# Performance work log

Measured on AMD Instinct MI355X. Metric: run time of the kernel, lower is better.

The kernel has to match this reference:

```python
import jax, jax.numpy as jnp
import numpy as np

N = 256          # Preisach mesh resolution
M = 4096         # number of applied-field time steps
H_MIN = -1.0
H_MAX = 1.0
B_SAT = 1.0


def setup_inputs() -> dict:
    key = jax.random.key(0)
    k1, k2 = jax.random.split(key)
    # applied magnetic field trace H_1..H_t in [0, 1)
    h = jax.random.uniform(k1, (M,), dtype=jnp.float32)
    # raw (pre-softplus) hysteresis density vector, length n(n+1)/2
    raw_density = jax.random.normal(k2, (N * (N + 1) // 2,), dtype=jnp.float32)
    # generate_asym_mesh equivalent: beta (xx) varies along columns,
    # alpha (yy) along rows; tril keeps the alpha >= beta Preisach triangle.
    lin = jnp.linspace(H_MIN, H_MAX, N, dtype=jnp.float32)
    xx, yy = jnp.meshgrid(lin, lin)
    return {"h": h, "raw_density": raw_density, "xx": xx, "yy": yy}


def _update_states(h, xx, yy):
    # hs = [-h_min, H_1, ..., H_t]
    hs = jnp.concatenate([jnp.full((1,), -H_MIN, dtype=h.dtype), h])
    # faithful to torch: at i=0, hs[i-1] wraps to the LAST element hs[-1]
    prev = jnp.concatenate([hs[-1:], hs[:-1]])
    init = -jnp.ones_like(xx)  # all hysterons start 'off'

    def step(state, hp_h):
        hp, hc = hp_h
        swept_up = jnp.where(yy >= hc, state, 1.0)    # sweep up: flip on below alpha=h
        swept_dn = jnp.where(xx <= hc, state, -1.0)   # sweep left: flip off above beta=h
        new = jnp.where(hc > hp, swept_up,
                        jnp.where(hc < hp, swept_dn, state))
        new = jnp.tril(new)
        return new, new

    _, states = jax.lax.scan(step, init, (prev, hs))
    return states  # (M+1, N, N)


def reference(h, raw_density, xx, yy):
    n = xx.shape[0]
    states = _update_states(h, xx, yy)
    # softplus density, scattered into lower-triangular matrix (vector_to_tril)
    dens_vec = jax.nn.softplus(raw_density)
    dens = jnp.zeros((n, n), dtype=dens_vec.dtype).at[jnp.tril_indices(n)].set(dens_vec)
    a = B_SAT / jnp.sum(dens)
    # b[i] = sum(dens * states[i+1])  -> single contraction over mesh dims
    b = jnp.einsum('tij,ij->t', states[1:], dens)
    return b * a
```

## Files before the change

kernel.cpp:

```cpp
#include <hip/hip_runtime.h>
#include <hip/hip_bf16.h>


#define NN 256
#define MM 4096
#define LSTEPS 16
#define NCHUNK (MM / LSTEPS)


__device__ __forceinline__ int rowOff(int i) { return i * (i + 3) / 2; }

__global__ __launch_bounds__(NN) void k_prep(const float* __restrict__ raw,
                                             const float* __restrict__ h,
                                             const float* __restrict__ lin,
                                             float* __restrict__ pref,
                                             int* __restrict__ codes,
                                             int* __restrict__ agg) {
    int tid = threadIdx.x;
    if (blockIdx.x < NN) {
        int i = blockIdx.x;
        float sp = 0.f;
        if (tid <= i) {
            float x = raw[i * (i + 1) / 2 + tid];
            sp = (x > 20.f) ? x : log1pf(expf(x));
        }
        float v = sp;
        int lane = tid & 63, wid = tid >> 6;
        #pragma unroll
        for (int o = 1; o < 64; o <<= 1) {
            float n = __shfl_up(v, o);
            if (lane >= o) v += n;
        }
        __shared__ float wsum[4];
        if (lane == 63) wsum[wid] = v;
        __syncthreads();
        float off = 0.f;
        for (int w = 0; w < wid; ++w) off += wsum[w];
        v += off;
        int base = rowOff(i);
        if (tid == 0) pref[base] = 0.f;
        if (tid <= i) pref[base + tid + 1] = v;
    } else {
        __shared__ float slin[NN];
        slin[tid] = lin[tid];
        __syncthreads();
        int k = (blockIdx.x - NN) * NN + tid;
        float hc = h[k];
        float hp = (k == 0) ? 1.0f : h[k - 1];
        double td = ((double)hc + 1.0) * 127.5;
        int code;
        if (hc > hp) {
            int g = (int)ceil(td);
            while (g < NN && slin[g] < hc) ++g;
            while (g > 0 && slin[g - 1] >= hc) --g;
            code = (g << 16) | 0xFFFF;
        } else if (hc < hp) {
            int g = (int)floor(td) + 1;
            while (g < NN && slin[g] <= hc) ++g;
            while (g > 0 && slin[g - 1] > hc) --g;
            code = g;
        } else {
            code = 0xFFFF;
        }
        codes[k] = code;
        int iup = code >> 16, jdn = code & 0xFFFF;
        #pragma unroll
        for (int m = 1; m < 16; m <<= 1) {
            iup = max(iup, __shfl_xor(iup, m));
            jdn = min(jdn, __shfl_xor(jdn, m));
        }
        if ((tid & 15) == 0) agg[k >> 4] = (iup << 16) | jdn;
    }
}

__global__ __launch_bounds__(NN) void k_main(const int* __restrict__ codes,
                                             const int* __restrict__ aggG,
                                             const float* __restrict__ pref,
                                             float* __restrict__ out) {
    __shared__ __align__(16) int sc[MM];
    __shared__ __align__(16) int sagg[NCHUNK];
    __shared__ float sPart[LSTEPS + 1][4];
    int tid = threadIdx.x;
    const int i = tid;
    const int T = blockIdx.x * LSTEPS;

    int base = rowOff(i);
    float rowtot = pref[base + i + 1];

    {
        const int4* g4 = (const int4*)codes;
        int4* d4 = (int4*)sc;
        #pragma unroll
        for (int u = 0; u < MM / 4 / NN; ++u) d4[tid + u * NN] = g4[tid + u * NN];
        sagg[tid] = aggG[tid];
    }
    __syncthreads();

    int runmin = i + 1;
    int c = (i == NN - 1) ? 0 : i + 1;
    bool done = (i == NN - 1);
    const int4* s4 = (const int4*)sc;
    const int4* a4 = (const int4*)sagg;
    const int jlim = blockIdx.x - 1;
    for (int jb = (jlim >> 4) << 4; jb >= 0; jb -= 16) {
        if (__all(done)) break;
        int4 A0 = a4[jb / 4 + 0];
        int4 A1 = a4[jb / 4 + 1];
        int4 A2 = a4[jb / 4 + 2];
        int4 A3 = a4[jb / 4 + 3];
        int ag[16] = { A0.x, A0.y, A0.z, A0.w, A1.x, A1.y, A1.z, A1.w,
                       A2.x, A2.y, A2.z, A2.w, A3.x, A3.y, A3.z, A3.w };
        #pragma unroll
        for (int u = 0; u < 16; ++u) if (jb + u > jlim) ag[u] = 0xFFFF;
        bool anyw = false; int bmin = 0xFFFF;
        #pragma unroll
        for (int u = 0; u < 16; ++u) {
            anyw = anyw || (!done && (i < (ag[u] >> 16)));
            bmin = min(bmin, ag[u] & 0xFFFF);
        }
        if (__any(anyw)) {
            #pragma unroll
            for (int u = 15; u >= 0; --u) {
                int a = ag[u];
                bool want = !done && (i < (a >> 16));
                if (__any(want)) {
                    int q = jb + u;
                    int4 w0 = s4[q * 4 + 0];
                    int4 w1 = s4[q * 4 + 1];
                    int4 w2 = s4[q * 4 + 2];
                    int4 w3 = s4[q * 4 + 3];
                    int cb[16] = { w0.x, w0.y, w0.z, w0.w, w1.x, w1.y, w1.z, w1.w,
                                   w2.x, w2.y, w2.z, w2.w, w3.x, w3.y, w3.z, w3.w };
                    #pragma unroll
                    for (int s = 15; s >= 0; --s) {
                        int code = cb[s];
                        bool cover = i < (code >> 16);
                        runmin = min(runmin, code & 0xFFFF);
                        c = (cover && !done) ? runmin : c;
                        done = done || cover;
                    }
                } else {
                    runmin = min(runmin, a & 0xFFFF);
                }
            }
        } else {
            runmin = min(runmin, bmin);
        }
    }
    if (!done) c = runmin;

    int4 f0 = s4[blockIdx.x * 4 + 0];
    int4 f1 = s4[blockIdx.x * 4 + 1];
    int4 f2 = s4[blockIdx.x * 4 + 2];
    int4 f3 = s4[blockIdx.x * 4 + 3];
    int fc[16] = { f0.x, f0.y, f0.z, f0.w, f1.x, f1.y, f1.z, f1.w,
                   f2.x, f2.y, f2.z, f2.w, f3.x, f3.y, f3.z, f3.w };
    float vals[LSTEPS];
    #pragma unroll
    for (int kk = 0; kk < LSTEPS; ++kk) {
        int code = fc[kk];
        c = (i < (code >> 16)) ? (i + 1) : min(c, code & 0xFFFF);
        vals[kk] = pref[base + c];
    }
    #pragma unroll
    for (int kk = 0; kk <= LSTEPS; ++kk) {
        float v = (kk < LSTEPS) ? vals[kk] : rowtot;
        v += __shfl_xor(v, 1);  v += __shfl_xor(v, 2);  v += __shfl_xor(v, 4);
        v += __shfl_xor(v, 8);  v += __shfl_xor(v, 16); v += __shfl_xor(v, 32);
        if ((tid & 63) == 0) sPart[kk][tid >> 6] = v;
    }
    __syncthreads();
    if (tid < LSTEPS) {
        float s  = sPart[tid][0] + sPart[tid][1] + sPart[tid][2] + sPart[tid][3];
        float st = sPart[LSTEPS][0] + sPart[LSTEPS][1] + sPart[LSTEPS][2] + sPart[LSTEPS][3];
        out[T + tid] = (2.f * s - st) / st;
    }
}

extern "C" void kernel_launch(void* const* d_in, const int* in_sizes, int n_in,
                              void* d_out, int out_size, void* d_ws, size_t ws_size,
                              hipStream_t stream) {
    const float* h   = (const float*)d_in[0];
    const float* raw = (const float*)d_in[1];
    const float* xx  = (const float*)d_in[2];

    int*   codes = (int*)d_ws;
    int*   agg   = (int*)((char*)d_ws + 16384);
    float* pref  = (float*)((char*)d_ws + 17408);

    k_prep<<<NN + MM / NN, NN, 0, stream>>>(raw, h, xx, pref, codes, agg);
    k_main<<<MM / LSTEPS, NN, 0, stream>>>(codes, agg, pref, (float*)d_out);
}
```

Baseline: 69.86 us.

## Replace backward scan with precomputed per-row composable chunk operators

Each row's state transition over a chunk of 16 steps is encoded as a composable operator (a reset flag plus a running min). The prep kernel precomputes these operators per chunk and per superchunk. The main kernel then composes at most about 31 operators to get the initial state. This replaces the data-dependent backward search with early exits, removes staging all 4096 codes into shared memory, and shrinks shared-memory use. The cost is extra global reads of the operator tables and more work in the prep kernel.

```diff
diff --git a/kernel.cpp b/kernel.cpp
--- a/kernel.cpp
+++ b/kernel.cpp
@@ -1,21 +1,29 @@
 #include <hip/hip_runtime.h>
-#include <hip/hip_bf16.h>
 
 
 #define NN 256
 #define MM 4096
 #define LSTEPS 16
 #define NCHUNK (MM / LSTEPS)
+#define NSUP   (NCHUNK / 16)
+#define IDENT  0xFFFF
 
 
 __device__ __forceinline__ int rowOff(int i) { return i * (i + 3) / 2; }
+
+__device__ __forceinline__ int opcompose(int a, int b) {
+    int m = min(a & 0xFFFF, b & 0xFFFF);
+    int r = (a & 0x10000) | m;
+    return (b & 0x10000) ? b : r;
+}
 
 __global__ __launch_bounds__(NN) void k_prep(const float* __restrict__ raw,
                                              const float* __restrict__ h,
                                              const float* __restrict__ lin,
                                              float* __restrict__ pref,
                                              int* __restrict__ codes,
-                                             int* __restrict__ agg) {
+                                             int* __restrict__ sup,
+                                             int4* __restrict__ cho) {
     int tid = threadIdx.x;
     if (blockIdx.x < NN) {
         int i = blockIdx.x;
@@ -42,9 +50,11 @@
         if (tid <= i) pref[base + tid + 1] = v;
     } else {
         __shared__ float slin[NN];
+        __shared__ __align__(16) int scodes[NN];
         slin[tid] = lin[tid];
         __syncthreads();
-        int k = (blockIdx.x - NN) * NN + tid;
+        int e = blockIdx.x - NN;
+        int k = e * NN + tid;
         float hc = h[k];
         float hp = (k == 0) ? 1.0f : h[k - 1];
         double td = ((double)hc + 1.0) * 127.5;
@@ -63,102 +73,84 @@
             code = 0xFFFF;
         }
         codes[k] = code;
-        int iup = code >> 16, jdn = code & 0xFFFF;
+        scodes[tid] = code;
+        __syncthreads();
+
+        const int i = tid;
+        const int4* s4 = (const int4*)scodes;
+        int cop[16];
         #pragma unroll
-        for (int m = 1; m < 16; m <<= 1) {
-            iup = max(iup, __shfl_xor(iup, m));
-            jdn = min(jdn, __shfl_xor(jdn, m));
+        for (int u = 0; u < 16; ++u) {
+            int4 q0 = s4[u * 4 + 0];
+            int4 q1 = s4[u * 4 + 1];
+            int4 q2 = s4[u * 4 + 2];
+            int4 q3 = s4[u * 4 + 3];
+            int cb[16] = { q0.x, q0.y, q0.z, q0.w, q1.x, q1.y, q1.z, q1.w,
+                           q2.x, q2.y, q2.z, q2.w, q3.x, q3.y, q3.z, q3.w };
+            int run = IDENT;
+            #pragma unroll
+            for (int s = 0; s < 16; ++s) {
+                int code = cb[s];
+                bool cov = i < (code >> 16);
+                int mn = (run & 0x10000) | min(run & 0xFFFF, code & 0xFFFF);
+                run = cov ? (0x10000 | (i + 1)) : mn;
+            }
+            cop[u] = run;
         }
-        if ((tid & 15) == 0) agg[k >> 4] = (iup << 16) | jdn;
+        int sop = IDENT;
+        #pragma unroll
+        for (int u = 0; u < 16; ++u) sop = opcompose(sop, cop[u]);
+        sup[e * NN + i] = sop;
+        #pragma unroll
+        for (int g = 0; g < 4; ++g)
+            cho[(e * 4 + g) * NN + i] =
+                make_int4(cop[4 * g + 0], cop[4 * g + 1], cop[4 * g + 2], cop[4 * g + 3]);
     }
 }
 
 __global__ __launch_bounds__(NN) void k_main(const int* __restrict__ codes,
-                                             const int* __restrict__ aggG,
+                                             const int* __restrict__ sup,
+                                             const int4* __restrict__ cho,
                                              const float* __restrict__ pref,
                                              float* __restrict__ out) {
-    __shared__ __align__(16) int sc[MM];
-    __shared__ __align__(16) int sagg[NCHUNK];
+    __shared__ int sc16[LSTEPS];
     __shared__ float sPart[LSTEPS + 1][4];
     int tid = threadIdx.x;
     const int i = tid;
-    const int T = blockIdx.x * LSTEPS;
+    const int b = blockIdx.x;
+    const int T = b * LSTEPS;
+    const int s = b >> 4;
+
+    if (tid < LSTEPS) sc16[tid] = codes[T + tid];
 
     int base = rowOff(i);
     float rowtot = pref[base + i + 1];
 
-    {
-        const int4* g4 = (const int4*)codes;
-        int4* d4 = (int4*)sc;
-        #pragma unroll
-        for (int u = 0; u < MM / 4 / NN; ++u) d4[tid + u * NN] = g4[tid + u * NN];
-        sagg[tid] = aggG[tid];
+    int run = IDENT;
+    #pragma unroll
+    for (int sp = 0; sp < NSUP - 1; ++sp) {
+        int v = sup[sp * NN + i];
+        run = opcompose(run, (sp < s) ? v : IDENT);
     }
+    #pragma unroll
+    for (int g = 0; g < 4; ++g) {
+        int4 q = cho[(s * 4 + g) * NN + i];
+        int C = s * 16 + g * 4;
+        run = opcompose(run, (C + 0 < b) ? q.x : IDENT);
+        run = opcompose(run, (C + 1 < b) ? q.y : IDENT);
+        run = opcompose(run, (C + 2 < b) ? q.z : IDENT);
+        run = opcompose(run, (C + 3 < b) ? q.w : IDENT);
+    }
+
+    int c = (i == NN - 1) ? 0 : i + 1;
+    { int m = run & 0xFFFF; c = (run & 0x10000) ? m : min(c, m); }
+
     __syncthreads();
 
-    int runmin = i + 1;
-    int c = (i == NN - 1) ? 0 : i + 1;
-    bool done = (i == NN - 1);
-    const int4* s4 = (const int4*)sc;
-    const int4* a4 = (const int4*)sagg;
-    const int jlim = blockIdx.x - 1;
-    for (int jb = (jlim >> 4) << 4; jb >= 0; jb -= 16) {
-        if (__all(done)) break;
-        int4 A0 = a4[jb / 4 + 0];
-        int4 A1 = a4[jb / 4 + 1];
-        int4 A2 = a4[jb / 4 + 2];
-        int4 A3 = a4[jb / 4 + 3];
-        int ag[16] = { A0.x, A0.y, A0.z, A0.w, A1.x, A1.y, A1.z, A1.w,
-                       A2.x, A2.y, A2.z, A2.w, A3.x, A3.y, A3.z, A3.w };
-        #pragma unroll
-        for (int u = 0; u < 16; ++u) if (jb + u > jlim) ag[u] = 0xFFFF;
-        bool anyw = false; int bmin = 0xFFFF;
-        #pragma unroll
-        for (int u = 0; u < 16; ++u) {
-            anyw = anyw || (!done && (i < (ag[u] >> 16)));
-            bmin = min(bmin, ag[u] & 0xFFFF);
-        }
-        if (__any(anyw)) {
-            #pragma unroll
-            for (int u = 15; u >= 0; --u) {
-                int a = ag[u];
-                bool want = !done && (i < (a >> 16));
-                if (__any(want)) {
-                    int q = jb + u;
-                    int4 w0 = s4[q * 4 + 0];
-                    int4 w1 = s4[q * 4 + 1];
-                    int4 w2 = s4[q * 4 + 2];
-                    int4 w3 = s4[q * 4 + 3];
-                    int cb[16] = { w0.x, w0.y, w0.z, w0.w, w1.x, w1.y, w1.z, w1.w,
-                                   w2.x, w2.y, w2.z, w2.w, w3.x, w3.y, w3.z, w3.w };
-                    #pragma unroll
-                    for (int s = 15; s >= 0; --s) {
-                        int code = cb[s];
-                        bool cover = i < (code >> 16);
-                        runmin = min(runmin, code & 0xFFFF);
-                        c = (cover && !done) ? runmin : c;
-                        done = done || cover;
-                    }
-                } else {
-                    runmin = min(runmin, a & 0xFFFF);
-                }
-            }
-        } else {
-            runmin = min(runmin, bmin);
-        }
-    }
-    if (!done) c = runmin;
-
-    int4 f0 = s4[blockIdx.x * 4 + 0];
-    int4 f1 = s4[blockIdx.x * 4 + 1];
-    int4 f2 = s4[blockIdx.x * 4 + 2];
-    int4 f3 = s4[blockIdx.x * 4 + 3];
-    int fc[16] = { f0.x, f0.y, f0.z, f0.w, f1.x, f1.y, f1.z, f1.w,
-                   f2.x, f2.y, f2.z, f2.w, f3.x, f3.y, f3.z, f3.w };
     float vals[LSTEPS];
     #pragma unroll
     for (int kk = 0; kk < LSTEPS; ++kk) {
-        int code = fc[kk];
+        int code = sc16[kk];
         c = (i < (code >> 16)) ? (i + 1) : min(c, code & 0xFFFF);
         vals[kk] = pref[base + c];
     }
@@ -171,9 +163,9 @@
     }
     __syncthreads();
     if (tid < LSTEPS) {
-        float s  = sPart[tid][0] + sPart[tid][1] + sPart[tid][2] + sPart[tid][3];
+        float sm = sPart[tid][0] + sPart[tid][1] + sPart[tid][2] + sPart[tid][3];
         float st = sPart[LSTEPS][0] + sPart[LSTEPS][1] + sPart[LSTEPS][2] + sPart[LSTEPS][3];
-        out[T + tid] = (2.f * s - st) / st;
+        out[T + tid] = (2.f * sm - st) / st;
     }
 }
 
@@ -185,9 +177,10 @@
     const float* xx  = (const float*)d_in[2];
 
     int*   codes = (int*)d_ws;
-    int*   agg   = (int*)((char*)d_ws + 16384);
-    float* pref  = (float*)((char*)d_ws + 17408);
+    int*   sup   = (int*)((char*)d_ws + 16384);
+    int4*  cho   = (int4*)((char*)d_ws + 32768);
+    float* pref  = (float*)((char*)d_ws + 294912);
 
-    k_prep<<<NN + MM / NN, NN, 0, stream>>>(raw, h, xx, pref, codes, agg);
-    k_main<<<MM / LSTEPS, NN, 0, stream>>>(codes, agg, pref, (float*)d_out);
+    k_prep<<<NN + MM / NN, NN, 0, stream>>>(raw, h, xx, pref, codes, sup, cho);
+    k_main<<<NCHUNK, NN, 0, stream>>>(codes, sup, cho, pref, (float*)d_out);
 }
```

New measurement: 69.36 us. Within noise of the previous version (-0.7%).
